# Kernel optimization log

Hardware: AMD Instinct MI355X
Metric: run time of the kernel (lower is better)

Reference implementation:

```python
import jax, jax.numpy as jnp
import numpy as np

RATIOS = np.array([0.5, 1.0, 2.0], np.float32)
SCALES = np.array([8.0, 16.0, 32.0], np.float32)
IMAGE_SIZE = 1920.0
UPPER, LOWER = 0.4, 0.1
NPOS_MAX, NNEG_MAX = 128, 60   # sample_num=256 -> bg_num = min(60, 256-npos) = 60
BETA = 0.1
EPS = 1e-6


def make_anchors(H, W, stride):
    # K = len(RATIOS)*len(SCALES) anchors per grid cell, sizes stride*scale, aspect per ratio
    ws = (stride * SCALES[None, :] * np.sqrt(1.0 / RATIOS[:, None])).reshape(-1)  # [K]
    hs = (stride * SCALES[None, :] * np.sqrt(RATIOS[:, None])).reshape(-1)        # [K]
    cx = (np.arange(W, dtype=np.float32) + 0.5) * stride
    cy = (np.arange(H, dtype=np.float32) + 0.5) * stride
    cxg, cyg = np.meshgrid(cx, cy)  # [H, W]
    a = np.stack([cxg[..., None] - ws / 2, cyg[..., None] - hs / 2,
                  cxg[..., None] + ws / 2, cyg[..., None] + hs / 2], axis=-1)  # [H, W, K, 4]
    return jnp.asarray(a, jnp.float32)


def pairwise_iou(b, g):
    # b: [A, 4], g: [M, 4] -> [A, M]
    ab = jnp.maximum(b[:, 2] - b[:, 0], 0.0) * jnp.maximum(b[:, 3] - b[:, 1], 0.0)
    ag = jnp.maximum(g[:, 2] - g[:, 0], 0.0) * jnp.maximum(g[:, 3] - g[:, 1], 0.0)
    x1 = jnp.maximum(b[:, None, 0], g[None, :, 0])
    y1 = jnp.maximum(b[:, None, 1], g[None, :, 1])
    x2 = jnp.minimum(b[:, None, 2], g[None, :, 2])
    y2 = jnp.minimum(b[:, None, 3], g[None, :, 3])
    inter = jnp.maximum(x2 - x1, 0.0) * jnp.maximum(y2 - y1, 0.0)
    return inter / (ab[:, None] + ag[None, :] - inter + EPS)


def encode(box, anchor):
    # standard (tx, ty, tw, th) box encoding relative to anchor
    aw = anchor[:, 2] - anchor[:, 0]; ah = anchor[:, 3] - anchor[:, 1]
    acx = anchor[:, 0] + 0.5 * aw; acy = anchor[:, 1] + 0.5 * ah
    bw = jnp.maximum(box[:, 2] - box[:, 0], EPS); bh = jnp.maximum(box[:, 3] - box[:, 1], EPS)
    bcx = box[:, 0] + 0.5 * bw; bcy = box[:, 1] + 0.5 * bh
    return jnp.stack([(bcx - acx) / aw, (bcy - acy) / ah,
                      jnp.log(bw / aw), jnp.log(bh / ah)], axis=-1)


def smooth_l1(d):
    ad = jnp.abs(d)
    return jnp.where(ad < BETA, 0.5 * d * d / BETA, ad - 0.5 * BETA)


def per_image(regions, cls, gt, key, anchors_flat, n_norm):
    iou = pairwise_iou(regions, gt)                       # [A, M]
    best = iou.max(axis=1)
    arg = iou.argmax(axis=1).astype(jnp.int32)
    # match(): >= upper -> gt index (positive), < lower -> NEGATIVE(-1), else ignore(-2)
    matches = jnp.where(best >= UPPER, arg, jnp.where(best < LOWER, -1, -2))
    kp, kn = jax.random.split(key)
    # randperm-style sampling without replacement: top_k over random scores on masked anchors
    pos_score = jnp.where(matches >= 0, jax.random.uniform(kp, matches.shape), -1.0)
    pv, pidx = jax.lax.top_k(pos_score, NPOS_MAX)
    pvalid = (pv > 0.0).astype(jnp.float32)               # npos = min(num_pos, 128)
    neg_score = jnp.where(matches == -1, jax.random.uniform(kn, matches.shape), -1.0)
    nv, nidx = jax.lax.top_k(neg_score, NNEG_MAX)
    nvalid = (nv > 0.0).astype(jnp.float32)
    npos = pvalid.sum(); nneg = nvalid.sum()
    lp = cls[pidx]; ln = cls[nidx]
    # BCEWithLogits(mean): label 1 -> softplus(-x), label 0 -> softplus(x)
    bce = jnp.sum(jax.nn.softplus(-lp) * pvalid) + jnp.sum(jax.nn.softplus(ln) * nvalid)
    denom = jnp.maximum(npos + nneg, 1.0)
    cls_loss = bce / denom
    gt_sel = gt[jnp.clip(matches[pidx], 0, gt.shape[0] - 1)]
    anc = anchors_flat[pidx]
    tp = encode(regions[pidx], anc)
    tg = encode(gt_sel, anc)
    l1 = smooth_l1(tp - tg).sum(-1)                       # [NPOS_MAX]
    bbox_loss = jnp.sum(l1 * pvalid) / (jnp.maximum(npos, 1.0) * n_norm)
    pred_mean = (jnp.sum(lp * pvalid) + jnp.sum(ln * nvalid)) / denom
    return cls_loss, bbox_loss, npos, nneg, pred_mean


def reference(cls_scores, bbox_deltas, gt_boxes):
    N, K, H, W = cls_scores.shape
    stride = round(IMAGE_SIZE / W)
    anc = make_anchors(H, W, stride)                      # [H, W, K, 4]
    deltas = bbox_deltas.transpose(0, 2, 3, 1).reshape(N, H, W, K, 4)
    # regions = anchors + deltas, cross_boundary(remove=False) -> clip to image
    regions = jnp.clip(anc[None] + deltas, 0.0, IMAGE_SIZE).reshape(N, -1, 4)
    cls = cls_scores.transpose(0, 2, 3, 1).reshape(N, -1)
    keys = jax.random.split(jax.random.key(42), N)
    cl, bl, fg, bg, pm = jax.vmap(per_image, in_axes=(0, 0, 0, 0, None, None))(
        regions, cls, gt_boxes, keys, anc.reshape(-1, 4), float(N))
    return (cl.sum(), bl.sum(), bg.sum(), fg.sum(), pm[-1])


def setup_inputs():
    key = jax.random.key(0)
    k1, k2, k3, k4 = jax.random.split(key, 4)
    N, K, H, W, M = 8, 9, 120, 120, 64
    cls_scores = jax.random.normal(k1, (N, K, H, W), jnp.float32)
    bbox_deltas = jax.random.normal(k2, (N, 4 * K, H, W), jnp.float32) * 4.0
    xy = jax.random.uniform(k3, (N, M, 2), jnp.float32) * 1500.0
    wh = jax.random.uniform(k4, (N, M, 2), jnp.float32) * 360.0 + 40.0
    gt_boxes = jnp.concatenate([xy, xy + wh], axis=-1)    # valid [x1,y1,x2,y2] in-image
    return {"cls_scores": cls_scores, "bbox_deltas": bbox_deltas, "gt_boxes": gt_boxes}
```

## Files before the change

kernel.cpp:

```cpp
#include <hip/hip_runtime.h>
#include <stdint.h>

#define N_IMG 8
#define K_ANC 9
#define HW_G  14400
#define W_G   120
#define A_TOT 129600
#define M_GT  64
#define NBIN  1024
#define CAP   2048
#define NSUB  8

static constexpr size_t OFF_PHIST = 0;
static constexpr size_t OFF_NHIST = 32768;
static constexpr size_t OFF_CNT   = 65536;
static constexpr size_t OFF_THR   = 65600;
static constexpr size_t OFF_ACC   = 65792;
static constexpr size_t ZERO_BYTES = 67328;
static constexpr size_t OFF_ENT   = 67584;
static constexpr size_t OFF_BND   = OFF_ENT + 4ull * N_IMG * A_TOT;

__device__ __forceinline__ uint32_t rotl32(uint32_t v, int r) {
  return (v << r) | (v >> (32 - r));
}

__device__ void tf2x32(uint32_t k0, uint32_t k1, uint32_t x0, uint32_t x1,
                       uint32_t& o0, uint32_t& o1) {
  uint32_t ks2 = 0x1BD11BDAu ^ k0 ^ k1;
  x0 += k0; x1 += k1;
#define TF_R(r) { x0 += x1; x1 = rotl32(x1, r); x1 ^= x0; }
  TF_R(13) TF_R(15) TF_R(26) TF_R(6)
  x0 += k1; x1 += ks2 + 1u;
  TF_R(17) TF_R(29) TF_R(16) TF_R(24)
  x0 += ks2; x1 += k0 + 2u;
  TF_R(13) TF_R(15) TF_R(26) TF_R(6)
  x0 += k0; x1 += k1 + 3u;
  TF_R(17) TF_R(29) TF_R(16) TF_R(24)
  x0 += k1; x1 += ks2 + 4u;
  TF_R(13) TF_R(15) TF_R(26) TF_R(6)
  x0 += ks2; x1 += k0 + 5u;
#undef TF_R
  o0 = x0; o1 = x1;
}

constexpr uint64_t tf_c(uint32_t k0, uint32_t k1, uint32_t x0, uint32_t x1) {
  const int R[20] = {13,15,26,6,17,29,16,24,13,15,26,6,17,29,16,24,13,15,26,6};
  uint32_t ks[3] = {k0, k1, 0x1BD11BDAu ^ k0 ^ k1};
  x0 += k0; x1 += k1;
  for (int r = 0; r < 20; ++r) {
    x0 += x1; x1 = (x1 << R[r]) | (x1 >> (32 - R[r])); x1 ^= x0;
    if ((r & 3) == 3) {
      int d = r / 4 + 1;
      x0 += ks[d % 3]; x1 += ks[(d + 1) % 3] + (uint32_t)d;
    }
  }
  return ((uint64_t)x0 << 32) | x1;
}

struct KeyTab { uint32_t v[N_IMG][4]; };
constexpr KeyTab make_keys() {
  KeyTab K{};
  for (int n = 0; n < N_IMG; ++n) {
    uint64_t f = tf_c(0u, 42u, 0u, (uint32_t)n);
    uint32_t i0 = (uint32_t)(f >> 32), i1 = (uint32_t)f;
    uint64_t p = tf_c(i0, i1, 0u, 0u);
    uint64_t q = tf_c(i0, i1, 0u, 1u);
    K.v[n][0] = (uint32_t)(p >> 32); K.v[n][1] = (uint32_t)p;
    K.v[n][2] = (uint32_t)(q >> 32); K.v[n][3] = (uint32_t)q;
  }
  return K;
}
__constant__ KeyTab KEYS = make_keys();

__device__ void acc_pos(int n, int l, int m, const float* __restrict__ cls,
                        const float* __restrict__ del, const float* __restrict__ gt,
                        float& sp, float& pr, float& l1s) {
  int k = l / HW_G, hw = l - k * HW_G;
  const float scales[3] = {8.f, 16.f, 32.f};
  const float ratios[3] = {0.5f, 1.f, 2.f};
  float sc = scales[k % 3], rt = ratios[k / 3];
  float wsz = (16.f * sc) * sqrtf(1.f / rt);
  float hsz = (16.f * sc) * sqrtf(rt);
  int w = hw % W_G, h = hw / W_G;
  float cx = ((float)w + 0.5f) * 16.f, cy = ((float)h + 0.5f) * 16.f;
  float ax1 = cx - wsz * 0.5f, ay1 = cy - hsz * 0.5f;
  float ax2 = cx + wsz * 0.5f, ay2 = cy + hsz * 0.5f;
  int base = (n * 36 + k * 4) * HW_G + hw;
  float rx1 = fminf(fmaxf(ax1 + del[base], 0.f), 1920.f);
  float ry1 = fminf(fmaxf(ay1 + del[base + HW_G], 0.f), 1920.f);
  float rx2 = fminf(fmaxf(ax2 + del[base + 2 * HW_G], 0.f), 1920.f);
  float ry2 = fminf(fmaxf(ay2 + del[base + 3 * HW_G], 0.f), 1920.f);
  float L = cls[n * A_TOT + l];
  sp += fmaxf(-L, 0.f) + log1pf(expf(-fabsf(L)));
  pr += L;
  const float* g = gt + (n * M_GT + m) * 4;
  float aw = ax2 - ax1, ah = ay2 - ay1;
  float acx = ax1 + 0.5f * aw, acy = ay1 + 0.5f * ah;
  float bw = fmaxf(rx2 - rx1, 1e-6f), bh = fmaxf(ry2 - ry1, 1e-6f);
  float bcx = rx1 + 0.5f * bw, bcy = ry1 + 0.5f * bh;
  float gw = fmaxf(g[2] - g[0], 1e-6f), gh = fmaxf(g[3] - g[1], 1e-6f);
  float gcx = g[0] + 0.5f * gw, gcy = g[1] + 0.5f * gh;
  float dd[4];
  dd[0] = (bcx - acx) / aw - (gcx - acx) / aw;
  dd[1] = (bcy - acy) / ah - (gcy - acy) / ah;
  dd[2] = logf(bw / aw) - logf(gw / aw);
  dd[3] = logf(bh / ah) - logf(gh / ah);
  float t = 0.f;
  for (int i = 0; i < 4; ++i) {
    float ad = fabsf(dd[i]);
    t += (ad < 0.1f) ? (0.5f * dd[i] * dd[i] / 0.1f) : (ad - 0.05f);
  }
  l1s += t;
}

__device__ void acc_neg(int n, int l, const float* __restrict__ cls,
                        float& sp, float& pr) {
  float L = cls[n * A_TOT + l];
  sp += fmaxf(L, 0.f) + log1pf(expf(-fabsf(L)));
  pr += L;
}

__device__ void reduce3_atomic(float sp, float pr, float l1, float* accf, int n,
                               int tid) {
  __shared__ float swv[3][4];
  float v0 = sp, v1 = pr, v2 = l1;
  for (int off = 32; off > 0; off >>= 1) {
    v0 += __shfl_down(v0, off); v1 += __shfl_down(v1, off); v2 += __shfl_down(v2, off);
  }
  int wv = tid >> 6, ln = tid & 63;
  if (ln == 0) { swv[0][wv] = v0; swv[1][wv] = v1; swv[2][wv] = v2; }
  __syncthreads();
  if (tid == 0) {
    atomicAdd(&accf[n * 48 + 0],  swv[0][0] + swv[0][1] + swv[0][2] + swv[0][3]);
    atomicAdd(&accf[n * 48 + 16], swv[1][0] + swv[1][1] + swv[1][2] + swv[1][3]);
    atomicAdd(&accf[n * 48 + 32], swv[2][0] + swv[2][1] + swv[2][2] + swv[2][3]);
  }
}

__global__ __launch_bounds__(64) void k_match(
    const float* __restrict__ del, const float* __restrict__ gt, uint8_t* ws) {
  const int k = blockIdx.y, n = blockIdx.z;
  const int tid = threadIdx.x;
  const int hw = blockIdx.x * 64 + tid;
  __shared__ float4 gbox[M_GT];
  __shared__ float gar[M_GT];
  {
    float4 b = reinterpret_cast<const float4*>(gt)[n * M_GT + tid];
    gbox[tid] = b;
    gar[tid] = fmaxf(b.z - b.x, 0.f) * fmaxf(b.w - b.y, 0.f);
  }
  __syncthreads();

  const float scales[3] = {8.f, 16.f, 32.f};
  const float ratios[3] = {0.5f, 1.f, 2.f};
  float sc = scales[k % 3], rt = ratios[k / 3];
  float wsz = (16.f * sc) * sqrtf(1.f / rt);
  float hsz = (16.f * sc) * sqrtf(rt);
  int w = hw % W_G, h = hw / W_G;
  float cx = ((float)w + 0.5f) * 16.f, cy = ((float)h + 0.5f) * 16.f;
  float ax1 = cx - wsz * 0.5f, ay1 = cy - hsz * 0.5f;
  float ax2 = cx + wsz * 0.5f, ay2 = cy + hsz * 0.5f;
  const float* dp = del + (size_t)(n * 36 + k * 4) * HW_G + hw;
  float rx1 = fminf(fmaxf(ax1 + dp[0], 0.f), 1920.f);
  float ry1 = fminf(fmaxf(ay1 + dp[HW_G], 0.f), 1920.f);
  float rx2 = fminf(fmaxf(ax2 + dp[2 * HW_G], 0.f), 1920.f);
  float ry2 = fminf(fmaxf(ay2 + dp[3 * HW_G], 0.f), 1920.f);
  float ab = fmaxf(rx2 - rx1, 0.f) * fmaxf(ry2 - ry1, 0.f);

  float ib = -1.f, ub = 1.f;
  int arg = 0;
#pragma unroll 8
  for (int j = 0; j < M_GT; ++j) {
    float4 b = gbox[j];
    float ix1 = fmaxf(rx1, b.x), iy1 = fmaxf(ry1, b.y);
    float ix2 = fminf(rx2, b.z), iy2 = fminf(ry2, b.w);
    float inter = fmaxf(ix2 - ix1, 0.f) * fmaxf(iy2 - iy1, 0.f);
    float u = ab + gar[j] - inter + 1e-6f;
    bool gc = (inter * ub) > (ib * u);
    ib = gc ? inter : ib;
    ub = gc ? u : ub;
    arg = gc ? j : arg;
  }
  float best = ib / ub;
  int m = (best >= 0.4f) ? arg : ((best < 0.1f) ? -1 : -2);

  uint32_t a32 = (uint32_t)(hw * 9 + k);
  uint32_t sk0 = (m >= 0) ? KEYS.v[n][0] : KEYS.v[n][2];
  uint32_t sk1 = (m >= 0) ? KEYS.v[n][1] : KEYS.v[n][3];
  uint32_t y0, y1;
  tf2x32(sk0, sk1, 0u, a32, y0, y1);
  uint32_t bits = (y0 ^ y1) >> 9;

  uint32_t e = 0u;
  if (bits) {
    if (m >= 0)       e = 0x80000000u | ((uint32_t)m << 23) | bits;
    else if (m == -1) e = bits;
  }
  ((uint32_t*)(ws + OFF_ENT))[(size_t)n * A_TOT + (size_t)k * HW_G + hw] = e;
  if (e) {
    uint32_t* hist = (uint32_t*)(ws + OFF_PHIST);
    uint32_t off = (e >> 31) ? 0u : (uint32_t)(N_IMG * NBIN);
    atomicAdd(&hist[off + n * NBIN + (bits >> 13)], 1u);
  }
}

__global__ __launch_bounds__(256) void k_scan(
    const float* __restrict__ cls, const float* __restrict__ del,
    const float* __restrict__ gt, uint8_t* ws) {
  const int sub = blockIdx.x, which = blockIdx.y, n = blockIdx.z;
  const int tid = threadIdx.x;
  const uint32_t* hist = (const uint32_t*)(ws + OFF_PHIST);
  const uint32_t* ent = (const uint32_t*)(ws + OFF_ENT);
  int* cnt = (int*)(ws + OFF_CNT);
  int* thrg = (int*)(ws + OFF_THR);
  unsigned long long* bnd = (unsigned long long*)(ws + OFF_BND);
  float* accf = (float*)(ws + OFF_ACC);

  __shared__ uint32_t shist[NBIN];
  __shared__ uint32_t chunk[256];
  __shared__ int tb[3];

  const uint32_t* hsrc = hist + (which ? (size_t)N_IMG * NBIN : 0) + n * NBIN;
  for (int i = tid; i < NBIN; i += 256) shist[i] = hsrc[i];
  __syncthreads();
  chunk[tid] = shist[tid * 4] + shist[tid * 4 + 1] +
               shist[tid * 4 + 2] + shist[tid * 4 + 3];
  __syncthreads();
  if (tid == 0) {
    int kk = (which == 0) ? 128 : 60;
    unsigned c = 0; int b = -1; int need = 0;
    for (int t = 255; t >= 0; --t) {
      unsigned cc = chunk[t];
      if (c + cc >= (unsigned)kk) {
        for (int i = t * 4 + 3;; --i) {
          unsigned hc = shist[i];
          if (c + hc >= (unsigned)kk) { b = i; need = kk - (int)c; break; }
          c += hc;
        }
        break;
      }
      c += cc;
    }
    tb[0] = b; tb[1] = need; tb[2] = (b < 0) ? (int)c : kk;
  }
  __syncthreads();
  if (sub == 0 && tid < 3) thrg[n * 6 + which * 3 + tid] = tb[tid];

  const int bB = tb[0];
  float sp = 0.f, pr = 0.f, l1 = 0.f;
  const uint32_t* en = ent + (size_t)n * A_TOT;

  for (int it = 0; it < 16; ++it) {
    int l0 = sub * 16384 + it * 1024 + tid * 4;
    if (l0 >= A_TOT) break;
    uint4 e4 = *reinterpret_cast<const uint4*>(en + l0);
    uint32_t ev[4] = {e4.x, e4.y, e4.z, e4.w};
#pragma unroll
    for (int j = 0; j < 4; ++j) {
      uint32_t e = ev[j];
      if (!e) continue;
      bool isPos = (e >> 31) != 0u;
      if ((which == 0) != isPos) continue;
      int l = l0 + j;
      uint32_t bits = e & 0x7FFFFFu;
      int bin = (int)(bits >> 13);
      if (bin > bB) {
        if (isPos) acc_pos(n, l, (int)((e >> 23) & 0x3Fu), cls, del, gt, sp, pr, l1);
        else       acc_neg(n, l, cls, sp, pr);
      } else if (bin == bB) {
        int i = atomicAdd(&cnt[n * 2 + which], 1);
        if (i < CAP) {
          int k = l / HW_G, hw = l - k * HW_G, a = hw * 9 + k;
          bnd[(size_t)(n * 2 + which) * CAP + i] =
              ((unsigned long long)bits << 17) | (unsigned)(0x1FFFF - a);
        }
      }
    }
  }
  reduce3_atomic(sp, pr, l1, accf, n, tid);
}

__global__ __launch_bounds__(256) void k_bound(
    const float* __restrict__ cls, const float* __restrict__ del,
    const float* __restrict__ gt, uint8_t* ws) {
  const int which = blockIdx.x, n = blockIdx.y, tid = threadIdx.x;
  const uint32_t* ent = (const uint32_t*)(ws + OFF_ENT);
  const int* thr = (const int*)(ws + OFF_THR);
  const int* cnt = (const int*)(ws + OFF_CNT);
  const unsigned long long* bnd =
      (const unsigned long long*)(ws + OFF_BND) + (size_t)(n * 2 + which) * CAP;
  float* accf = (float*)(ws + OFF_ACC);

  int need = thr[n * 6 + which * 3 + 1];
  float sp = 0.f, pr = 0.f, l1 = 0.f;
  if (need > 0) {
    __shared__ unsigned long long sb[CAP];
    int m = min(cnt[n * 2 + which], CAP);
    for (int i = tid; i < m; i += 256) sb[i] = bnd[i];
    __syncthreads();
    for (int i = tid; i < m; i += 256) {
      unsigned long long key = sb[i];
      int rank = 0;
      for (int j = 0; j < m; ++j) rank += (sb[j] > key) ? 1 : 0;
      if (rank < need) {
        int a = 0x1FFFF - (int)(key & 0x1FFFFull);
        int k = a % 9, hw = a / 9;
        int l = k * HW_G + hw;
        if (which == 0) {
          uint32_t e = ent[(size_t)n * A_TOT + l];
          acc_pos(n, l, (int)((e >> 23) & 0x3Fu), cls, del, gt, sp, pr, l1);
        } else {
          acc_neg(n, l, cls, sp, pr);
        }
      }
    }
    __syncthreads();
  }
  reduce3_atomic(sp, pr, l1, accf, n, tid);
}

__global__ __launch_bounds__(64) void k_out(float* __restrict__ out, uint8_t* ws) {
  if (threadIdx.x != 0) return;
  const int* thr = (const int*)(ws + OFF_THR);
  const float* acc = (const float*)(ws + OFF_ACC);
  float c = 0.f, b = 0.f, fg = 0.f, bg = 0.f, pm = 0.f;
  for (int n = 0; n < N_IMG; ++n) {
    float npos = (float)thr[n * 6 + 2];
    float nneg = (float)thr[n * 6 + 5];
    float denom = fmaxf(npos + nneg, 1.f);
    c += acc[n * 48 + 0] / denom;
    b += acc[n * 48 + 32] / (fmaxf(npos, 1.f) * 8.0f);
    fg += npos; bg += nneg;
    if (n == N_IMG - 1) pm = acc[n * 48 + 16] / denom;
  }
  out[0] = c; out[1] = b; out[2] = bg; out[3] = fg; out[4] = pm;
}

extern "C" void kernel_launch(void* const* d_in, const int* in_sizes, int n_in,
                              void* d_out, int out_size, void* d_ws, size_t ws_size,
                              hipStream_t stream) {
  (void)in_sizes; (void)n_in; (void)out_size; (void)ws_size;
  const float* cls = (const float*)d_in[0];
  const float* del = (const float*)d_in[1];
  const float* gt  = (const float*)d_in[2];
  float* out = (float*)d_out;
  uint8_t* ws = (uint8_t*)d_ws;

  hipMemsetAsync(ws, 0, ZERO_BYTES, stream);
  hipLaunchKernelGGL(k_match, dim3(HW_G / 64, K_ANC, N_IMG), dim3(64), 0, stream,
                     del, gt, ws);
  hipLaunchKernelGGL(k_scan, dim3(NSUB, 2, N_IMG), dim3(256), 0, stream,
                     cls, del, gt, ws);
  hipLaunchKernelGGL(k_bound, dim3(2, N_IMG), dim3(256), 0, stream,
                     cls, del, gt, ws);
  hipLaunchKernelGGL(k_out, dim3(1), dim3(64), 0, stream, out, ws);
}
```

Measured before the change: 149.3 us.

## Fuse scan, boundary and output kernels via last-block-done atomics; widen match blocks

Merges the scan, boundary-selection and final output kernels into one kernel. The last sub-block of each group, detected with an atomic counter and thread fences, does the boundary ranking, and the last group overall writes the final outputs. This removes two kernel launches and the gaps between them. k_match also moves from 64-thread to 256-thread blocks with a bounds check, so the gt boxes are loaded once per 256 anchors instead of once per 64. The cost is that the boundary work is serialized behind the slowest sub-block, and correctness now depends on the fence and counter ordering.

```diff
diff --git a/kernel.cpp b/kernel.cpp
--- a/kernel.cpp
+++ b/kernel.cpp
@@ -15,8 +15,10 @@
 static constexpr size_t OFF_NHIST = 32768;
 static constexpr size_t OFF_CNT   = 65536;
 static constexpr size_t OFF_THR   = 65600;
-static constexpr size_t OFF_ACC   = 65792;
-static constexpr size_t ZERO_BYTES = 67328;
+static constexpr size_t OFF_GCNT  = 65792;
+static constexpr size_t OFF_DONE  = 65856;
+static constexpr size_t OFF_ACC   = 65920;
+static constexpr size_t ZERO_BYTES = 67456;
 static constexpr size_t OFF_ENT   = 67584;
 static constexpr size_t OFF_BND   = OFF_ENT + 4ull * N_IMG * A_TOT;
 
@@ -135,21 +137,23 @@
     atomicAdd(&accf[n * 48 + 16], swv[1][0] + swv[1][1] + swv[1][2] + swv[1][3]);
     atomicAdd(&accf[n * 48 + 32], swv[2][0] + swv[2][1] + swv[2][2] + swv[2][3]);
   }
-}
-
-__global__ __launch_bounds__(64) void k_match(
+  __syncthreads();
+}
+
+__global__ __launch_bounds__(256, 8) void k_match(
     const float* __restrict__ del, const float* __restrict__ gt, uint8_t* ws) {
   const int k = blockIdx.y, n = blockIdx.z;
   const int tid = threadIdx.x;
-  const int hw = blockIdx.x * 64 + tid;
+  const int hw = blockIdx.x * 256 + tid;
   __shared__ float4 gbox[M_GT];
   __shared__ float gar[M_GT];
-  {
+  if (tid < M_GT) {
     float4 b = reinterpret_cast<const float4*>(gt)[n * M_GT + tid];
     gbox[tid] = b;
     gar[tid] = fmaxf(b.z - b.x, 0.f) * fmaxf(b.w - b.y, 0.f);
   }
   __syncthreads();
+  if (hw >= HW_G) return;
 
   const float scales[3] = {8.f, 16.f, 32.f};
   const float ratios[3] = {0.5f, 1.f, 2.f};
@@ -204,52 +208,58 @@
   }
 }
 
-__global__ __launch_bounds__(256) void k_scan(
+__global__ __launch_bounds__(256) void k_tail(
     const float* __restrict__ cls, const float* __restrict__ del,
-    const float* __restrict__ gt, uint8_t* ws) {
+    const float* __restrict__ gt, float* __restrict__ out, uint8_t* ws) {
   const int sub = blockIdx.x, which = blockIdx.y, n = blockIdx.z;
   const int tid = threadIdx.x;
+  const int grp = which * N_IMG + n;
   const uint32_t* hist = (const uint32_t*)(ws + OFF_PHIST);
   const uint32_t* ent = (const uint32_t*)(ws + OFF_ENT);
   int* cnt = (int*)(ws + OFF_CNT);
   int* thrg = (int*)(ws + OFF_THR);
+  uint32_t* gcnt = (uint32_t*)(ws + OFF_GCNT);
+  uint32_t* done = (uint32_t*)(ws + OFF_DONE);
   unsigned long long* bnd = (unsigned long long*)(ws + OFF_BND);
   float* accf = (float*)(ws + OFF_ACC);
 
-  __shared__ uint32_t shist[NBIN];
-  __shared__ uint32_t chunk[256];
+  __shared__ __align__(16) unsigned char smem[16384];
   __shared__ int tb[3];
-
-  const uint32_t* hsrc = hist + (which ? (size_t)N_IMG * NBIN : 0) + n * NBIN;
-  for (int i = tid; i < NBIN; i += 256) shist[i] = hsrc[i];
-  __syncthreads();
-  chunk[tid] = shist[tid * 4] + shist[tid * 4 + 1] +
-               shist[tid * 4 + 2] + shist[tid * 4 + 3];
-  __syncthreads();
-  if (tid == 0) {
-    int kk = (which == 0) ? 128 : 60;
-    unsigned c = 0; int b = -1; int need = 0;
-    for (int t = 255; t >= 0; --t) {
-      unsigned cc = chunk[t];
-      if (c + cc >= (unsigned)kk) {
-        for (int i = t * 4 + 3;; --i) {
-          unsigned hc = shist[i];
-          if (c + hc >= (unsigned)kk) { b = i; need = kk - (int)c; break; }
-          c += hc;
+  __shared__ int sFlag;
+
+  {
+    uint32_t* shist = (uint32_t*)smem;
+    uint32_t* chunk = (uint32_t*)(smem + 4096);
+    const uint32_t* hsrc = hist + (which ? (size_t)N_IMG * NBIN : 0) + n * NBIN;
+    for (int i = tid; i < NBIN; i += 256) shist[i] = hsrc[i];
+    __syncthreads();
+    chunk[tid] = shist[tid * 4] + shist[tid * 4 + 1] +
+                 shist[tid * 4 + 2] + shist[tid * 4 + 3];
+    __syncthreads();
+    if (tid == 0) {
+      int kk = (which == 0) ? 128 : 60;
+      unsigned c = 0; int b = -1; int need = 0;
+      for (int t = 255; t >= 0; --t) {
+        unsigned cc = chunk[t];
+        if (c + cc >= (unsigned)kk) {
+          for (int i = t * 4 + 3;; --i) {
+            unsigned hc = shist[i];
+            if (c + hc >= (unsigned)kk) { b = i; need = kk - (int)c; break; }
+            c += hc;
+          }
+          break;
         }
-        break;
+        c += cc;
       }
-      c += cc;
-    }
-    tb[0] = b; tb[1] = need; tb[2] = (b < 0) ? (int)c : kk;
-  }
-  __syncthreads();
-  if (sub == 0 && tid < 3) thrg[n * 6 + which * 3 + tid] = tb[tid];
+      tb[0] = b; tb[1] = need; tb[2] = (b < 0) ? (int)c : kk;
+    }
+    __syncthreads();
+    if (sub == 0 && tid < 3) thrg[n * 6 + which * 3 + tid] = tb[tid];
+  }
 
   const int bB = tb[0];
   float sp = 0.f, pr = 0.f, l1 = 0.f;
   const uint32_t* en = ent + (size_t)n * A_TOT;
-
   for (int it = 0; it < 16; ++it) {
     int l0 = sub * 16384 + it * 1024 + tid * 4;
     if (l0 >= A_TOT) break;
@@ -278,62 +288,62 @@
     }
   }
   reduce3_atomic(sp, pr, l1, accf, n, tid);
-}
-
-__global__ __launch_bounds__(256) void k_bound(
-    const float* __restrict__ cls, const float* __restrict__ del,
-    const float* __restrict__ gt, uint8_t* ws) {
-  const int which = blockIdx.x, n = blockIdx.y, tid = threadIdx.x;
-  const uint32_t* ent = (const uint32_t*)(ws + OFF_ENT);
-  const int* thr = (const int*)(ws + OFF_THR);
-  const int* cnt = (const int*)(ws + OFF_CNT);
-  const unsigned long long* bnd =
-      (const unsigned long long*)(ws + OFF_BND) + (size_t)(n * 2 + which) * CAP;
-  float* accf = (float*)(ws + OFF_ACC);
-
-  int need = thr[n * 6 + which * 3 + 1];
-  float sp = 0.f, pr = 0.f, l1 = 0.f;
-  if (need > 0) {
-    __shared__ unsigned long long sb[CAP];
-    int m = min(cnt[n * 2 + which], CAP);
-    for (int i = tid; i < m; i += 256) sb[i] = bnd[i];
-    __syncthreads();
-    for (int i = tid; i < m; i += 256) {
-      unsigned long long key = sb[i];
-      int rank = 0;
-      for (int j = 0; j < m; ++j) rank += (sb[j] > key) ? 1 : 0;
-      if (rank < need) {
-        int a = 0x1FFFF - (int)(key & 0x1FFFFull);
-        int k = a % 9, hw = a / 9;
-        int l = k * HW_G + hw;
-        if (which == 0) {
-          uint32_t e = ent[(size_t)n * A_TOT + l];
-          acc_pos(n, l, (int)((e >> 23) & 0x3Fu), cls, del, gt, sp, pr, l1);
-        } else {
-          acc_neg(n, l, cls, sp, pr);
+
+  __threadfence();
+  if (tid == 0) sFlag = (atomicAdd(&gcnt[grp], 1u) == NSUB - 1) ? 1 : 0;
+  __syncthreads();
+  if (!sFlag) return;
+  __threadfence();
+
+  {
+    int need = tb[1];
+    float sp2 = 0.f, pr2 = 0.f, l12 = 0.f;
+    if (need > 0) {
+      unsigned long long* sb = (unsigned long long*)smem;
+      const unsigned long long* bsrc = bnd + (size_t)(n * 2 + which) * CAP;
+      int m = min(cnt[n * 2 + which], CAP);
+      for (int i = tid; i < m; i += 256) sb[i] = bsrc[i];
+      __syncthreads();
+      for (int i = tid; i < m; i += 256) {
+        unsigned long long key = sb[i];
+        int rank = 0;
+        for (int j = 0; j < m; ++j) rank += (sb[j] > key) ? 1 : 0;
+        if (rank < need) {
+          int a = 0x1FFFF - (int)(key & 0x1FFFFull);
+          int k = a % 9, hw = a / 9;
+          int l = k * HW_G + hw;
+          if (which == 0) {
+            uint32_t e = ent[(size_t)n * A_TOT + l];
+            acc_pos(n, l, (int)((e >> 23) & 0x3Fu), cls, del, gt, sp2, pr2, l12);
+          } else {
+            acc_neg(n, l, cls, sp2, pr2);
+          }
         }
       }
-    }
-    __syncthreads();
-  }
-  reduce3_atomic(sp, pr, l1, accf, n, tid);
-}
-
-__global__ __launch_bounds__(64) void k_out(float* __restrict__ out, uint8_t* ws) {
-  if (threadIdx.x != 0) return;
-  const int* thr = (const int*)(ws + OFF_THR);
-  const float* acc = (const float*)(ws + OFF_ACC);
-  float c = 0.f, b = 0.f, fg = 0.f, bg = 0.f, pm = 0.f;
-  for (int n = 0; n < N_IMG; ++n) {
-    float npos = (float)thr[n * 6 + 2];
-    float nneg = (float)thr[n * 6 + 5];
-    float denom = fmaxf(npos + nneg, 1.f);
-    c += acc[n * 48 + 0] / denom;
-    b += acc[n * 48 + 32] / (fmaxf(npos, 1.f) * 8.0f);
-    fg += npos; bg += nneg;
-    if (n == N_IMG - 1) pm = acc[n * 48 + 16] / denom;
-  }
-  out[0] = c; out[1] = b; out[2] = bg; out[3] = fg; out[4] = pm;
+      __syncthreads();
+    }
+    reduce3_atomic(sp2, pr2, l12, accf, n, tid);
+  }
+
+  __threadfence();
+  if (tid == 0) sFlag = (atomicAdd(done, 1u) == 2 * N_IMG - 1) ? 1 : 0;
+  __syncthreads();
+  if (!sFlag) return;
+  __threadfence();
+
+  if (tid == 0) {
+    float c = 0.f, b = 0.f, fg = 0.f, bg = 0.f, pm = 0.f;
+    for (int nn = 0; nn < N_IMG; ++nn) {
+      float npos = (float)thrg[nn * 6 + 2];
+      float nneg = (float)thrg[nn * 6 + 5];
+      float denom = fmaxf(npos + nneg, 1.f);
+      c += accf[nn * 48 + 0] / denom;
+      b += accf[nn * 48 + 32] / (fmaxf(npos, 1.f) * 8.0f);
+      fg += npos; bg += nneg;
+      if (nn == N_IMG - 1) pm = accf[nn * 48 + 16] / denom;
+    }
+    out[0] = c; out[1] = b; out[2] = bg; out[3] = fg; out[4] = pm;
+  }
 }
 
 extern "C" void kernel_launch(void* const* d_in, const int* in_sizes, int n_in,
@@ -347,11 +357,8 @@
   uint8_t* ws = (uint8_t*)d_ws;
 
   hipMemsetAsync(ws, 0, ZERO_BYTES, stream);
-  hipLaunchKernelGGL(k_match, dim3(HW_G / 64, K_ANC, N_IMG), dim3(64), 0, stream,
-                     del, gt, ws);
-  hipLaunchKernelGGL(k_scan, dim3(NSUB, 2, N_IMG), dim3(256), 0, stream,
-                     cls, del, gt, ws);
-  hipLaunchKernelGGL(k_bound, dim3(2, N_IMG), dim3(256), 0, stream,
-                     cls, del, gt, ws);
-  hipLaunchKernelGGL(k_out, dim3(1), dim3(64), 0, stream, out, ws);
-}
+  hipLaunchKernelGGL(k_match, dim3((HW_G + 255) / 256, K_ANC, N_IMG), dim3(256),
+                     0, stream, del, gt, ws);
+  hipLaunchKernelGGL(k_tail, dim3(NSUB, 2, N_IMG), dim3(256), 0, stream,
+                     cls, del, gt, out, ws);
+}
```

Measured after the change: 153.0 us. 2.4% more time.

## Cull GT boxes per wavefront in matching and fold output into bound kernel

Applied to the files above, without the earlier changes.

In k_match, each 64-thread wave reduces the bounding extent of its 64 proposal boxes and compacts only the ground-truth boxes that overlap that extent into shared memory. It then loops over just those candidates, keeping the original GT index for the argmax. This cuts the per-anchor IoU loop when proposals are spatially clustered. Separately, the final output kernel is merged into k_bound via a last-block-done atomic counter, saving one launch at the cost of extra fences and a done counter in the workspace.

```diff
diff --git a/kernel.cpp b/kernel.cpp
--- a/kernel.cpp
+++ b/kernel.cpp
@@ -15,8 +15,9 @@
 static constexpr size_t OFF_NHIST = 32768;
 static constexpr size_t OFF_CNT   = 65536;
 static constexpr size_t OFF_THR   = 65600;
-static constexpr size_t OFF_ACC   = 65792;
-static constexpr size_t ZERO_BYTES = 67328;
+static constexpr size_t OFF_DONE  = 65856;
+static constexpr size_t OFF_ACC   = 65920;
+static constexpr size_t ZERO_BYTES = 67456;
 static constexpr size_t OFF_ENT   = 67584;
 static constexpr size_t OFF_BND   = OFF_ENT + 4ull * N_IMG * A_TOT;
 
@@ -135,6 +136,7 @@
     atomicAdd(&accf[n * 48 + 16], swv[1][0] + swv[1][1] + swv[1][2] + swv[1][3]);
     atomicAdd(&accf[n * 48 + 32], swv[2][0] + swv[2][1] + swv[2][2] + swv[2][3]);
   }
+  __syncthreads();
 }
 
 __global__ __launch_bounds__(64) void k_match(
@@ -142,14 +144,11 @@
   const int k = blockIdx.y, n = blockIdx.z;
   const int tid = threadIdx.x;
   const int hw = blockIdx.x * 64 + tid;
-  __shared__ float4 gbox[M_GT];
-  __shared__ float gar[M_GT];
-  {
-    float4 b = reinterpret_cast<const float4*>(gt)[n * M_GT + tid];
-    gbox[tid] = b;
-    gar[tid] = fmaxf(b.z - b.x, 0.f) * fmaxf(b.w - b.y, 0.f);
-  }
-  __syncthreads();
+  __shared__ float4 cbox[M_GT];
+  __shared__ float car[M_GT];
+  __shared__ int cidx[M_GT];
+
+  float4 g4 = reinterpret_cast<const float4*>(gt)[n * M_GT + tid];
 
   const float scales[3] = {8.f, 16.f, 32.f};
   const float ratios[3] = {0.5f, 1.f, 2.f};
@@ -167,19 +166,37 @@
   float ry2 = fminf(fmaxf(ay2 + dp[3 * HW_G], 0.f), 1920.f);
   float ab = fmaxf(rx2 - rx1, 0.f) * fmaxf(ry2 - ry1, 0.f);
 
+  float xmn = rx1, xmx = rx2, ymn = ry1, ymx = ry2;
+  for (int off = 32; off > 0; off >>= 1) {
+    xmn = fminf(xmn, __shfl_xor(xmn, off));
+    xmx = fmaxf(xmx, __shfl_xor(xmx, off));
+    ymn = fminf(ymn, __shfl_xor(ymn, off));
+    ymx = fmaxf(ymx, __shfl_xor(ymx, off));
+  }
+  bool keep = (g4.x < xmx) && (g4.z > xmn) && (g4.y < ymx) && (g4.w > ymn);
+  unsigned long long mk = __ballot(keep);
+  int Mp = __popcll(mk);
+  if (keep) {
+    int pos = __popcll(mk & ((1ull << tid) - 1ull));
+    cbox[pos] = g4;
+    car[pos] = fmaxf(g4.z - g4.x, 0.f) * fmaxf(g4.w - g4.y, 0.f);
+    cidx[pos] = tid;
+  }
+
   float ib = -1.f, ub = 1.f;
   int arg = 0;
-#pragma unroll 8
-  for (int j = 0; j < M_GT; ++j) {
-    float4 b = gbox[j];
+  for (int j = 0; j < Mp; ++j) {
+    float4 b = cbox[j];
+    float ga = car[j];
+    int oj = cidx[j];
     float ix1 = fmaxf(rx1, b.x), iy1 = fmaxf(ry1, b.y);
     float ix2 = fminf(rx2, b.z), iy2 = fminf(ry2, b.w);
     float inter = fmaxf(ix2 - ix1, 0.f) * fmaxf(iy2 - iy1, 0.f);
-    float u = ab + gar[j] - inter + 1e-6f;
+    float u = ab + ga - inter + 1e-6f;
     bool gc = (inter * ub) > (ib * u);
     ib = gc ? inter : ib;
     ub = gc ? u : ub;
-    arg = gc ? j : arg;
+    arg = gc ? oj : arg;
   }
   float best = ib / ub;
   int m = (best >= 0.4f) ? arg : ((best < 0.1f) ? -1 : -2);
@@ -249,7 +266,6 @@
   const int bB = tb[0];
   float sp = 0.f, pr = 0.f, l1 = 0.f;
   const uint32_t* en = ent + (size_t)n * A_TOT;
-
   for (int it = 0; it < 16; ++it) {
     int l0 = sub * 16384 + it * 1024 + tid * 4;
     if (l0 >= A_TOT) break;
@@ -280,9 +296,9 @@
   reduce3_atomic(sp, pr, l1, accf, n, tid);
 }
 
-__global__ __launch_bounds__(256) void k_bound(
+__global__ __launch_bounds__(256) void k_bound_out(
     const float* __restrict__ cls, const float* __restrict__ del,
-    const float* __restrict__ gt, uint8_t* ws) {
+    const float* __restrict__ gt, float* __restrict__ out, uint8_t* ws) {
   const int which = blockIdx.x, n = blockIdx.y, tid = threadIdx.x;
   const uint32_t* ent = (const uint32_t*)(ws + OFF_ENT);
   const int* thr = (const int*)(ws + OFF_THR);
@@ -290,6 +306,8 @@
   const unsigned long long* bnd =
       (const unsigned long long*)(ws + OFF_BND) + (size_t)(n * 2 + which) * CAP;
   float* accf = (float*)(ws + OFF_ACC);
+  uint32_t* done = (uint32_t*)(ws + OFF_DONE);
+  __shared__ int sLast;
 
   int need = thr[n * 6 + which * 3 + 1];
   float sp = 0.f, pr = 0.f, l1 = 0.f;
@@ -317,23 +335,27 @@
     __syncthreads();
   }
   reduce3_atomic(sp, pr, l1, accf, n, tid);
-}
-
-__global__ __launch_bounds__(64) void k_out(float* __restrict__ out, uint8_t* ws) {
-  if (threadIdx.x != 0) return;
-  const int* thr = (const int*)(ws + OFF_THR);
-  const float* acc = (const float*)(ws + OFF_ACC);
-  float c = 0.f, b = 0.f, fg = 0.f, bg = 0.f, pm = 0.f;
-  for (int n = 0; n < N_IMG; ++n) {
-    float npos = (float)thr[n * 6 + 2];
-    float nneg = (float)thr[n * 6 + 5];
-    float denom = fmaxf(npos + nneg, 1.f);
-    c += acc[n * 48 + 0] / denom;
-    b += acc[n * 48 + 32] / (fmaxf(npos, 1.f) * 8.0f);
-    fg += npos; bg += nneg;
-    if (n == N_IMG - 1) pm = acc[n * 48 + 16] / denom;
-  }
-  out[0] = c; out[1] = b; out[2] = bg; out[3] = fg; out[4] = pm;
+
+  __threadfence();
+  if (tid == 0) sLast = (atomicAdd(done, 1u) == 2u * N_IMG - 1u) ? 1 : 0;
+  __syncthreads();
+  if (!sLast) return;
+  __threadfence();
+
+  if (tid == 0) {
+    const int* thrr = (const int*)(ws + OFF_THR);
+    float c = 0.f, b = 0.f, fg = 0.f, bg = 0.f, pm = 0.f;
+    for (int nn = 0; nn < N_IMG; ++nn) {
+      float npos = (float)thrr[nn * 6 + 2];
+      float nneg = (float)thrr[nn * 6 + 5];
+      float denom = fmaxf(npos + nneg, 1.f);
+      c += accf[nn * 48 + 0] / denom;
+      b += accf[nn * 48 + 32] / (fmaxf(npos, 1.f) * 8.0f);
+      fg += npos; bg += nneg;
+      if (nn == N_IMG - 1) pm = accf[nn * 48 + 16] / denom;
+    }
+    out[0] = c; out[1] = b; out[2] = bg; out[3] = fg; out[4] = pm;
+  }
 }
 
 extern "C" void kernel_launch(void* const* d_in, const int* in_sizes, int n_in,
@@ -351,7 +373,6 @@
                      del, gt, ws);
   hipLaunchKernelGGL(k_scan, dim3(NSUB, 2, N_IMG), dim3(256), 0, stream,
                      cls, del, gt, ws);
-  hipLaunchKernelGGL(k_bound, dim3(2, N_IMG), dim3(256), 0, stream,
-                     cls, del, gt, ws);
-  hipLaunchKernelGGL(k_out, dim3(1), dim3(64), 0, stream, out, ws);
-}
+  hipLaunchKernelGGL(k_bound_out, dim3(2, N_IMG), dim3(256), 0, stream,
+                     cls, del, gt, out, ws);
+}
```

Result: faster. 132.8 us (-11.1%).
